# Kernel optimization log

Measured on AMD Instinct MI355X. Metric: run time of the kernel, lower is better.

## Reference

```python
import jax, jax.numpy as jnp
import numpy as np

B, N, E = 8, 2048, 2048  # requires N == E (see bmm(value, attn^T) constraint)

def setup_inputs() -> dict:
    key = jax.random.key(0)
    k1, k2, k3 = jax.random.split(key, 3)
    inputs = jax.random.normal(k1, (B, N, E), dtype=jnp.float32)
    # nn.Linear(embed_size, embed_size): weight [E,E], bias [E]
    W = jax.random.normal(k2, (E, E), dtype=jnp.float32) * (1.0 / np.sqrt(E))
    b = jax.random.normal(k3, (E,), dtype=jnp.float32) * 0.01
    gamma = jnp.zeros((), dtype=jnp.float32)  # nn.Parameter(torch.tensor(0.0))
    return {"inputs": inputs, "W": W, "b": b, "gamma": gamma}

def reference(inputs, W, b, gamma):
    # query = Linear(inputs); key = value = inputs
    query = jnp.einsum('bne,fe->bnf', inputs, W) + b          # [B,N,E]
    # scores = bmm(query, key^T) + gamma  -> [B,N,N]
    scores = jnp.einsum('bne,bme->bnm', query, inputs) + gamma
    # softmax over dim=1 (rows, NOT the usual last dim)
    attn = jax.nn.softmax(scores, axis=1)                      # [B,N,N]
    # output = bmm(value, attn^T): out[b,n,m] = sum_e value[b,n,e]*attn[b,m,e]
    out = jnp.einsum('bne,bme->bnm', inputs, attn)             # [B,N,N]
    return out
```

## Files before the change

### kernel.cpp

```cpp
#include <hip/hip_runtime.h>
#include <stdint.h>


typedef _Float16 f16;
typedef f16 f16x8 __attribute__((ext_vector_type(8)));
typedef f16 f16x4 __attribute__((ext_vector_type(4)));
typedef float f32x4 __attribute__((ext_vector_type(4)));

#define ND 2048
#define NNL 4194304L
#define NT 32

static __device__ __forceinline__ void stage16(const void* g, void* l) {
  __builtin_amdgcn_global_load_lds(
      (const __attribute__((address_space(1))) uint32_t*)g,
      (__attribute__((address_space(3))) uint32_t*)l, 16, 0, 0);
}

__global__ void cvt_f16(const float* __restrict__ x, f16* __restrict__ h, int n4) {
  int i = blockIdx.x * 256 + threadIdx.x;
  if (i >= n4) return;
  float4 v = reinterpret_cast<const float4*>(x)[i];
  f16x4 o;
  o.x = (f16)v.x; o.y = (f16)v.y; o.z = (f16)v.z; o.w = (f16)v.w;
  reinterpret_cast<f16x4*>(h)[i] = o;
}

#define RB(d_, o_, kh_) ((((d_) << 2) | ((o_) << 1) | (kh_)) * 16384)

#define STG(gp_, ro_, t_, kh_)                                           \
  do {                                                                   \
    stage16((gp_) + (long)(t_) * 128 + (kh_) * 64, smem + (ro_) + ld0);  \
    stage16((gp_) + 524288L + (long)(t_) * 128 + (kh_) * 64,             \
            smem + (ro_) + ld1);                                         \
  } while (0)

#define FENCE asm volatile("" ::: "memory")

#define SYNC(vm_)                                                        \
  do {                                                                   \
    asm volatile("s_waitcnt vmcnt(" #vm_ ") lgkmcnt(0)" ::: "memory");   \
    __builtin_amdgcn_s_barrier();                                        \
    FENCE;                                                               \
  } while (0)

#define PHASE(d_, mh_, kh_, RDB_, STAGE_)                                     \
  do {                                                                        \
    const char* ra_ = smem + RB(d_, 0, kh_) + (mh_) * 4096 + aoff;            \
    f16x8 af[4];                                                              \
    af[0] = *(const f16x8*)(ra_);                                             \
    af[1] = *(const f16x8*)(ra_ + 1024);                                      \
    af[2] = *(const f16x8*)(ra_ + 2048);                                      \
    af[3] = *(const f16x8*)(ra_ + 3072);                                      \
    if (RDB_) {                                                               \
      const char* rb_ = smem + RB(d_, 1, kh_) + boff;                         \
      bf[0] = *(const f16x8*)(rb_);                                           \
      bf[1] = *(const f16x8*)(rb_ + 1024);                                    \
      bf[2] = *(const f16x8*)(rb_ + 2048);                                    \
      bf[3] = *(const f16x8*)(rb_ + 3072);                                    \
    }                                                                         \
    STAGE_                                                                    \
    __builtin_amdgcn_s_setprio(1);                                            \
    _Pragma("unroll") for (int mt_ = 0; mt_ < 4; ++mt_) {                     \
      _Pragma("unroll") for (int nt_ = 0; nt_ < 4; ++nt_) {                   \
        acc[(mh_) * 4 + mt_][nt_] = __builtin_amdgcn_mfma_f32_16x16x32_f16(   \
            af[mt_], bf[nt_], acc[(mh_) * 4 + mt_][nt_], 0, 0, 0);            \
      }                                                                       \
    }                                                                         \
    __builtin_amdgcn_s_setprio(0);                                            \
  } while (0)

template <int MODE>
__launch_bounds__(512, 2) __global__
void gemm256(const f16* __restrict__ A, long sA, const f16* __restrict__ B, long sB,
             const float* __restrict__ bias, const float* __restrict__ gamma,
             float* __restrict__ Cf, f16* __restrict__ Ch) {
  __shared__ char smem[131072];

  const int bz = blockIdx.z;
  const long tm = (long)blockIdx.y * 256;
  const long tn = (long)blockIdx.x * 256;
  const int tid = threadIdx.x;
  const int lane = tid & 63;
  const int wid = tid >> 6;
  const int wm = (wid >> 2) << 7;
  const int wn = (wid & 3) << 6;

  const int sg = (tid & 3) ^ ((tid >> 3) & 3);
  const char* gA = (const char*)(A + bz * sA + tm * ND) + (long)(tid >> 2) * 4096 + sg * 16;
  const char* gB = (const char*)(B + bz * sB + tn * ND) + (long)(tid >> 2) * 4096 + sg * 16;
  const uint32_t ld0 = tid * 16u;
  const uint32_t ld1 = 8192u + tid * 16u;

  const int segsw = (((lane >> 4) ^ ((lane >> 1) & 3)) << 4);
  const int lrow = lane & 15;
  const int aoff = (wm + lrow) * 64 + segsw;
  const int boff = (wn + lrow) * 64 + segsw;

  f32x4 acc[8][4] = {};
  f16x8 bf[4];

  STG(gA, RB(0, 0, 0), 0, 0);
  STG(gB, RB(0, 1, 0), 0, 0);
  STG(gA, RB(0, 0, 1), 0, 1);
  STG(gB, RB(0, 1, 1), 0, 1);
  STG(gA, RB(1, 0, 0), 1, 0);
  STG(gB, RB(1, 1, 0), 1, 0);
  asm volatile("s_waitcnt vmcnt(8)" ::: "memory");
  __builtin_amdgcn_s_barrier();
  FENCE;

#pragma unroll 2
  for (int t = 0; t < NT - 2; ++t) {
    const int d = t & 1;
    const int e = d ^ 1;
    PHASE(d, 0, 0, 1, STG(gA, RB(e, 0, 1), t + 1, 1););
    PHASE(d, 1, 0, 0, STG(gB, RB(e, 1, 1), t + 1, 1););
    SYNC(8);
    PHASE(d, 0, 1, 1, STG(gA, RB(d, 0, 0), t + 2, 0););
    PHASE(d, 1, 1, 0, STG(gB, RB(d, 1, 0), t + 2, 0););
    SYNC(8);
  }
  {
    PHASE(0, 0, 0, 1, STG(gA, RB(1, 0, 1), NT - 1, 1););
    PHASE(0, 1, 0, 0, STG(gB, RB(1, 1, 1), NT - 1, 1););
    SYNC(8);
    PHASE(0, 0, 1, 1, ;);
    PHASE(0, 1, 1, 0, ;);
    SYNC(4);
  }
  {
    PHASE(1, 0, 0, 1, ;);
    PHASE(1, 1, 0, 0, ;);
    SYNC(0);
    PHASE(1, 0, 1, 1, ;);
    PHASE(1, 1, 1, 0, ;);
  }

  const int rr = (lane >> 4) << 2;
  const int cc = lane & 15;
  const long cb = (long)bz * NNL;
  if constexpr (MODE == 1) {
#pragma unroll
    for (int nt = 0; nt < 4; ++nt) {
      const long col = tn + wn + nt * 16 + cc;
      const float bj = bias[col];
#pragma unroll
      for (int mt = 0; mt < 8; ++mt) {
#pragma unroll
        for (int r = 0; r < 4; ++r) {
          const long row = tm + wm + mt * 16 + rr + r;
          Ch[cb + row * ND + col] = (f16)(acc[mt][nt][r] + bj);
        }
      }
    }
  } else {
    const float g = gamma ? gamma[0] : 0.0f;
#pragma unroll
    for (int mt = 0; mt < 8; ++mt) {
#pragma unroll
      for (int nt = 0; nt < 4; ++nt) {
#pragma unroll
        for (int r = 0; r < 4; ++r) {
          const long row = tm + wm + mt * 16 + rr + r;
          const long col = tn + wn + nt * 16 + cc;
          Cf[cb + row * ND + col] = acc[mt][nt][r] + g;
        }
      }
    }
  }
}

__global__ void stats_partial(const float* __restrict__ S, float* __restrict__ Mp,
                              float* __restrict__ Sp) {
  const int col = blockIdx.x * 256 + threadIdx.x;
  const int seg = blockIdx.y;
  const int b = blockIdx.z;
  const float* p = S + (long)b * NNL + (long)seg * 256 * ND + col;
  float m = -3.4e38f, s = 0.f;
  for (int n = 0; n < 256; ++n) {
    float x = p[(long)n * ND];
    float nm = fmaxf(m, x);
    s = s * __expf(m - nm) + __expf(x - nm);
    m = nm;
  }
  const long o = ((long)b * 8 + seg) * ND + col;
  Mp[o] = m;
  Sp[o] = s;
}

__global__ void stats_combine(const float* __restrict__ Mp, const float* __restrict__ Sp,
                              float* __restrict__ Mx, float* __restrict__ Rs) {
  const int col = blockIdx.x * 256 + threadIdx.x;
  const int b = blockIdx.y;
  float m = -3.4e38f, s = 0.f;
  for (int k = 0; k < 8; ++k) {
    const long o = ((long)b * 8 + k) * ND + col;
    float mk = Mp[o], sk = Sp[o];
    float nm = fmaxf(m, mk);
    s = s * __expf(m - nm) + sk * __expf(mk - nm);
    m = nm;
  }
  Mx[(long)b * ND + col] = m;
  Rs[(long)b * ND + col] = 1.0f / s;
}

__global__ void scale_exp_kernel(const float* __restrict__ S, const float* __restrict__ Mx,
                                 const float* __restrict__ Rs, f16* __restrict__ A) {
  const long i4 = (long)blockIdx.x * 256 + threadIdx.x;
  const long i = i4 * 4;
  const int b = (int)(i >> 22);
  const int col = (int)(i & 2047);
  float4 s = reinterpret_cast<const float4*>(S)[i4];
  float4 m4 = *reinterpret_cast<const float4*>(&Mx[(long)b * ND + col]);
  float4 r4 = *reinterpret_cast<const float4*>(&Rs[(long)b * ND + col]);
  f16x4 o;
  o.x = (f16)(__expf(s.x - m4.x) * r4.x);
  o.y = (f16)(__expf(s.y - m4.y) * r4.y);
  o.z = (f16)(__expf(s.z - m4.z) * r4.z);
  o.w = (f16)(__expf(s.w - m4.w) * r4.w);
  reinterpret_cast<f16x4*>(A)[i4] = o;
}

extern "C" void kernel_launch(void* const* d_in, const int* in_sizes, int n_in,
                              void* d_out, int out_size, void* d_ws, size_t ws_size,
                              hipStream_t stream) {
  (void)in_sizes; (void)n_in; (void)out_size;
  const float* X = (const float*)d_in[0];
  const float* W = (const float*)d_in[1];
  const float* bias = (const float*)d_in[2];
  const float* gamma = (const float*)d_in[3];

  char* ws = (char*)d_ws;
  f16* Xh = (f16*)(ws);
  f16* Wh = (f16*)(ws + 67108864L);
  f16* Qh = (f16*)(ws + 75497472L);
  float* S = (float*)(ws + 142606336L);
  float* Mp = (float*)(ws + 276824064L);
  float* Sp = (float*)(ws + 277348352L);
  float* Mx = (float*)(ws + 277872640L);
  float* Rs = (float*)(ws + 277938176L);
  f16* Amat = Qh;
  if (ws_size < 278003712UL) return;

  cvt_f16<<<32768, 256, 0, stream>>>(X, Xh, 8388608);
  cvt_f16<<<4096, 256, 0, stream>>>(W, Wh, 1048576);

  dim3 gg(8, 8, 8), bb(512);
  gemm256<1><<<gg, bb, 0, stream>>>(Xh, NNL, Wh, 0L, bias, nullptr, nullptr, Qh);
  gemm256<0><<<gg, bb, 0, stream>>>(Qh, NNL, Xh, NNL, nullptr, gamma, S, nullptr);
  stats_partial<<<dim3(8, 8, 8), 256, 0, stream>>>(S, Mp, Sp);
  stats_combine<<<dim3(8, 8), 256, 0, stream>>>(Mp, Sp, Mx, Rs);
  scale_exp_kernel<<<32768, 256, 0, stream>>>(S, Mx, Rs, Amat);
  gemm256<0><<<gg, bb, 0, stream>>>(Xh, NNL, Amat, NNL, nullptr, nullptr,
                                    (float*)d_out, nullptr);
}
```

Before: 692.9 us.

## Switch GEMM to 32x32x16 MFMA and fuse column softmax stats into scores GEMM

Replaces the 16x16x32 MFMA tiling with 32x32x16 MFMA (fewer instructions and fewer LDS fragment reads per K step, with a new swizzled fragment layout and epilogue row mapping). Adds a MODE 2 epilogue to the scores GEMM that computes per-column partial max and sum-exp over the 256-row tile through cross-lane shuffles and LDS, and drops the separate stats_partial kernel that re-read the whole scores matrix. The cost is extra epilogue work and barriers inside the GEMM, plus a risk of layout or indexing mistakes in the new fragment mapping.

```diff
diff --git a/kernel.cpp b/kernel.cpp
--- a/kernel.cpp
+++ b/kernel.cpp
@@ -6,6 +6,7 @@
 typedef f16 f16x8 __attribute__((ext_vector_type(8)));
 typedef f16 f16x4 __attribute__((ext_vector_type(4)));
 typedef float f32x4 __attribute__((ext_vector_type(4)));
+typedef float f32x16 __attribute__((ext_vector_type(16)));
 
 #define ND 2048
 #define NNL 4194304L
@@ -44,29 +45,33 @@
     FENCE;                                                               \
   } while (0)
 
-#define PHASE(d_, mh_, kh_, RDB_, STAGE_)                                     \
+#define MFMA32(a_, b_, c_) \
+  __builtin_amdgcn_mfma_f32_32x32x16_f16(a_, b_, c_, 0, 0, 0)
+
+#define PHASE32(d_, p_, kh_, RDB_, STAGE_)                                    \
   do {                                                                        \
-    const char* ra_ = smem + RB(d_, 0, kh_) + (mh_) * 4096 + aoff;            \
-    f16x8 af[4];                                                              \
-    af[0] = *(const f16x8*)(ra_);                                             \
-    af[1] = *(const f16x8*)(ra_ + 1024);                                      \
-    af[2] = *(const f16x8*)(ra_ + 2048);                                      \
-    af[3] = *(const f16x8*)(ra_ + 3072);                                      \
+    const char* ab_ = smem + RB(d_, 0, kh_) + (p_) * 4096;                    \
+    f16x8 af0 = *(const f16x8*)(ab_ + aoff0);                                 \
+    f16x8 af1 = *(const f16x8*)(ab_ + aoff1);                                 \
+    f16x8 af2 = *(const f16x8*)(ab_ + aoff0 + 2048);                          \
+    f16x8 af3 = *(const f16x8*)(ab_ + aoff1 + 2048);                          \
     if (RDB_) {                                                               \
-      const char* rb_ = smem + RB(d_, 1, kh_) + boff;                         \
-      bf[0] = *(const f16x8*)(rb_);                                           \
-      bf[1] = *(const f16x8*)(rb_ + 1024);                                    \
-      bf[2] = *(const f16x8*)(rb_ + 2048);                                    \
-      bf[3] = *(const f16x8*)(rb_ + 3072);                                    \
+      const char* bb_ = smem + RB(d_, 1, kh_);                                \
+      bf[0] = *(const f16x8*)(bb_ + boff0);                                   \
+      bf[1] = *(const f16x8*)(bb_ + boff1);                                   \
+      bf[2] = *(const f16x8*)(bb_ + boff0 + 2048);                            \
+      bf[3] = *(const f16x8*)(bb_ + boff1 + 2048);                            \
     }                                                                         \
     STAGE_                                                                    \
     __builtin_amdgcn_s_setprio(1);                                            \
-    _Pragma("unroll") for (int mt_ = 0; mt_ < 4; ++mt_) {                     \
-      _Pragma("unroll") for (int nt_ = 0; nt_ < 4; ++nt_) {                   \
-        acc[(mh_) * 4 + mt_][nt_] = __builtin_amdgcn_mfma_f32_16x16x32_f16(   \
-            af[mt_], bf[nt_], acc[(mh_) * 4 + mt_][nt_], 0, 0, 0);            \
-      }                                                                       \
-    }                                                                         \
+    acc[(p_)*2][0]   = MFMA32(af0, bf[0], acc[(p_)*2][0]);                    \
+    acc[(p_)*2][0]   = MFMA32(af1, bf[1], acc[(p_)*2][0]);                    \
+    acc[(p_)*2][1]   = MFMA32(af0, bf[2], acc[(p_)*2][1]);                    \
+    acc[(p_)*2][1]   = MFMA32(af1, bf[3], acc[(p_)*2][1]);                    \
+    acc[(p_)*2+1][0] = MFMA32(af2, bf[0], acc[(p_)*2+1][0]);                  \
+    acc[(p_)*2+1][0] = MFMA32(af3, bf[1], acc[(p_)*2+1][0]);                  \
+    acc[(p_)*2+1][1] = MFMA32(af2, bf[2], acc[(p_)*2+1][1]);                  \
+    acc[(p_)*2+1][1] = MFMA32(af3, bf[3], acc[(p_)*2+1][1]);                  \
     __builtin_amdgcn_s_setprio(0);                                            \
   } while (0)
 
@@ -74,7 +79,8 @@
 __launch_bounds__(512, 2) __global__
 void gemm256(const f16* __restrict__ A, long sA, const f16* __restrict__ B, long sB,
              const float* __restrict__ bias, const float* __restrict__ gamma,
-             float* __restrict__ Cf, f16* __restrict__ Ch) {
+             float* __restrict__ Cf, f16* __restrict__ Ch,
+             float* __restrict__ Mp, float* __restrict__ Sp) {
   __shared__ char smem[131072];
 
   const int bz = blockIdx.z;
@@ -92,12 +98,16 @@
   const uint32_t ld0 = tid * 16u;
   const uint32_t ld1 = 8192u + tid * 16u;
 
-  const int segsw = (((lane >> 4) ^ ((lane >> 1) & 3)) << 4);
-  const int lrow = lane & 15;
-  const int aoff = (wm + lrow) * 64 + segsw;
-  const int boff = (wn + lrow) * 64 + segsw;
-
-  f32x4 acc[8][4] = {};
+  const int r31 = lane & 31;
+  const int hi = lane >> 5;
+  const int axor = (r31 >> 1) & 3;
+  const int segk0 = ((hi ^ axor) << 4);
+  const int aoff0 = (wm + r31) * 64 + segk0;
+  const int aoff1 = aoff0 ^ 0x20;
+  const int boff0 = (wn + r31) * 64 + segk0;
+  const int boff1 = boff0 ^ 0x20;
+
+  f32x16 acc[4][2] = {};
   f16x8 bf[4];
 
   STG(gA, RB(0, 0, 0), 0, 0);
@@ -114,79 +124,112 @@
   for (int t = 0; t < NT - 2; ++t) {
     const int d = t & 1;
     const int e = d ^ 1;
-    PHASE(d, 0, 0, 1, STG(gA, RB(e, 0, 1), t + 1, 1););
-    PHASE(d, 1, 0, 0, STG(gB, RB(e, 1, 1), t + 1, 1););
+    PHASE32(d, 0, 0, 1, STG(gA, RB(e, 0, 1), t + 1, 1););
+    PHASE32(d, 1, 0, 0, STG(gB, RB(e, 1, 1), t + 1, 1););
     SYNC(8);
-    PHASE(d, 0, 1, 1, STG(gA, RB(d, 0, 0), t + 2, 0););
-    PHASE(d, 1, 1, 0, STG(gB, RB(d, 1, 0), t + 2, 0););
+    PHASE32(d, 0, 1, 1, STG(gA, RB(d, 0, 0), t + 2, 0););
+    PHASE32(d, 1, 1, 0, STG(gB, RB(d, 1, 0), t + 2, 0););
     SYNC(8);
   }
   {
-    PHASE(0, 0, 0, 1, STG(gA, RB(1, 0, 1), NT - 1, 1););
-    PHASE(0, 1, 0, 0, STG(gB, RB(1, 1, 1), NT - 1, 1););
+    PHASE32(0, 0, 0, 1, STG(gA, RB(1, 0, 1), NT - 1, 1););
+    PHASE32(0, 1, 0, 0, STG(gB, RB(1, 1, 1), NT - 1, 1););
     SYNC(8);
-    PHASE(0, 0, 1, 1, ;);
-    PHASE(0, 1, 1, 0, ;);
+    PHASE32(0, 0, 1, 1, ;);
+    PHASE32(0, 1, 1, 0, ;);
     SYNC(4);
   }
   {
-    PHASE(1, 0, 0, 1, ;);
-    PHASE(1, 1, 0, 0, ;);
+    PHASE32(1, 0, 0, 1, ;);
+    PHASE32(1, 1, 0, 0, ;);
     SYNC(0);
-    PHASE(1, 0, 1, 1, ;);
-    PHASE(1, 1, 1, 0, ;);
-  }
-
-  const int rr = (lane >> 4) << 2;
-  const int cc = lane & 15;
+    PHASE32(1, 0, 1, 1, ;);
+    PHASE32(1, 1, 1, 0, ;);
+  }
+
   const long cb = (long)bz * NNL;
   if constexpr (MODE == 1) {
 #pragma unroll
-    for (int nt = 0; nt < 4; ++nt) {
-      const long col = tn + wn + nt * 16 + cc;
+    for (int nt = 0; nt < 2; ++nt) {
+      const long col = tn + wn + nt * 32 + r31;
       const float bj = bias[col];
 #pragma unroll
-      for (int mt = 0; mt < 8; ++mt) {
-#pragma unroll
-        for (int r = 0; r < 4; ++r) {
-          const long row = tm + wm + mt * 16 + rr + r;
+      for (int mt = 0; mt < 4; ++mt) {
+#pragma unroll
+        for (int r = 0; r < 16; ++r) {
+          const long row = tm + wm + mt * 32 + (r & 3) + 8 * (r >> 2) + 4 * hi;
           Ch[cb + row * ND + col] = (f16)(acc[mt][nt][r] + bj);
         }
       }
     }
-  } else {
+  } else if constexpr (MODE == 0) {
     const float g = gamma ? gamma[0] : 0.0f;
 #pragma unroll
-    for (int mt = 0; mt < 8; ++mt) {
-#pragma unroll
-      for (int nt = 0; nt < 4; ++nt) {
-#pragma unroll
-        for (int r = 0; r < 4; ++r) {
-          const long row = tm + wm + mt * 16 + rr + r;
-          const long col = tn + wn + nt * 16 + cc;
+    for (int nt = 0; nt < 2; ++nt) {
+      const long col = tn + wn + nt * 32 + r31;
+#pragma unroll
+      for (int mt = 0; mt < 4; ++mt) {
+#pragma unroll
+        for (int r = 0; r < 16; ++r) {
+          const long row = tm + wm + mt * 32 + (r & 3) + 8 * (r >> 2) + 4 * hi;
           Cf[cb + row * ND + col] = acc[mt][nt][r] + g;
         }
       }
     }
-  }
-}
-
-__global__ void stats_partial(const float* __restrict__ S, float* __restrict__ Mp,
-                              float* __restrict__ Sp) {
-  const int col = blockIdx.x * 256 + threadIdx.x;
-  const int seg = blockIdx.y;
-  const int b = blockIdx.z;
-  const float* p = S + (long)b * NNL + (long)seg * 256 * ND + col;
-  float m = -3.4e38f, s = 0.f;
-  for (int n = 0; n < 256; ++n) {
-    float x = p[(long)n * ND];
-    float nm = fmaxf(m, x);
-    s = s * __expf(m - nm) + __expf(x - nm);
-    m = nm;
-  }
-  const long o = ((long)b * 8 + seg) * ND + col;
-  Mp[o] = m;
-  Sp[o] = s;
+  } else {
+    const float g = gamma[0];
+    __syncthreads();
+    float* redm = (float*)smem;
+    float* reds = redm + 512;
+#pragma unroll
+    for (int nt = 0; nt < 2; ++nt) {
+      float ml = -3.4e38f;
+#pragma unroll
+      for (int mt = 0; mt < 4; ++mt)
+#pragma unroll
+        for (int r = 0; r < 16; ++r)
+          ml = fmaxf(ml, acc[mt][nt][r] + g);
+      float sl = 0.f;
+#pragma unroll
+      for (int mt = 0; mt < 4; ++mt)
+#pragma unroll
+        for (int r = 0; r < 16; ++r)
+          sl += __expf(acc[mt][nt][r] + g - ml);
+      float pm = __shfl(ml, lane ^ 32, 64);
+      float ps = __shfl(sl, lane ^ 32, 64);
+      float m2 = fmaxf(ml, pm);
+      float s2 = sl * __expf(ml - m2) + ps * __expf(pm - m2);
+      if (hi == 0) {
+        redm[(wid * 2 + nt) * 32 + r31] = m2;
+        reds[(wid * 2 + nt) * 32 + r31] = s2;
+      }
+    }
+    __syncthreads();
+    if (tid < 256) {
+      const int g4 = tid >> 6, nt2 = (tid >> 5) & 1, l5 = tid & 31;
+      const float mA = redm[(g4 * 2 + nt2) * 32 + l5];
+      const float sA = reds[(g4 * 2 + nt2) * 32 + l5];
+      const float mB = redm[((4 + g4) * 2 + nt2) * 32 + l5];
+      const float sB = reds[((4 + g4) * 2 + nt2) * 32 + l5];
+      const float m = fmaxf(mA, mB);
+      const float s = sA * __expf(mA - m) + sB * __expf(mB - m);
+      const long o = ((long)bz * 8 + blockIdx.y) * ND + tn + tid;
+      Mp[o] = m;
+      Sp[o] = s;
+    }
+#pragma unroll
+    for (int nt = 0; nt < 2; ++nt) {
+      const long col = tn + wn + nt * 32 + r31;
+#pragma unroll
+      for (int mt = 0; mt < 4; ++mt) {
+#pragma unroll
+        for (int r = 0; r < 16; ++r) {
+          const long row = tm + wm + mt * 32 + (r & 3) + 8 * (r >> 2) + 4 * hi;
+          Cf[cb + row * ND + col] = acc[mt][nt][r] + g;
+        }
+      }
+    }
+  }
 }
 
 __global__ void stats_combine(const float* __restrict__ Mp, const float* __restrict__ Sp,
@@ -247,11 +290,12 @@
   cvt_f16<<<4096, 256, 0, stream>>>(W, Wh, 1048576);
 
   dim3 gg(8, 8, 8), bb(512);
-  gemm256<1><<<gg, bb, 0, stream>>>(Xh, NNL, Wh, 0L, bias, nullptr, nullptr, Qh);
-  gemm256<0><<<gg, bb, 0, stream>>>(Qh, NNL, Xh, NNL, nullptr, gamma, S, nullptr);
-  stats_partial<<<dim3(8, 8, 8), 256, 0, stream>>>(S, Mp, Sp);
+  gemm256<1><<<gg, bb, 0, stream>>>(Xh, NNL, Wh, 0L, bias, nullptr, nullptr, Qh,
+                                    nullptr, nullptr);
+  gemm256<2><<<gg, bb, 0, stream>>>(Qh, NNL, Xh, NNL, nullptr, gamma, S, nullptr,
+                                    Mp, Sp);
   stats_combine<<<dim3(8, 8), 256, 0, stream>>>(Mp, Sp, Mx, Rs);
   scale_exp_kernel<<<32768, 256, 0, stream>>>(S, Mx, Rs, Amat);
   gemm256<0><<<gg, bb, 0, stream>>>(Xh, NNL, Amat, NNL, nullptr, nullptr,
-                                    (float*)d_out, nullptr);
-}
+                                    (float*)d_out, nullptr, nullptr, nullptr);
+}
```

Measured after the change: 705.5 us. About the same (+1.8%).
